# Performance work log

Measured on AMD Instinct MI355X. Metric: run time of the kernel, lower is better.

The kernel has to match this reference:

```python
import jax, jax.numpy as jnp
import numpy as np

N_AGENTS = 32
N_HEADS = 8
HEAD_DIM = 32          # atten_dim // n_heads
HID = 256              # rnn_hidden_dim
ATT = 256              # atten_dim
N_ACT = 32
NEG = -1e9             # finite stand-in for -inf; exp underflows to 0 in softmax


def setup_inputs() -> dict:
    key = jax.random.key(0)
    ks = jax.random.split(key, 20)
    B, N, E = 4096, 64, 128
    w = lambda k, shape: (jax.random.normal(k, shape, jnp.float32) * 0.05)
    return {
        "inputs": jax.random.normal(ks[0], (B, N, E), jnp.float32),
        "hidden_state": jax.random.normal(ks[1], (B, N_AGENTS, HID), jnp.float32) * 0.1,
        "fc1_w": w(ks[2], (HID, E)), "fc1_b": jnp.zeros((HID,), jnp.float32),
        "q_w": w(ks[3], (ATT, HID)), "q_b": jnp.zeros((ATT,), jnp.float32),
        "k_w": w(ks[4], (ATT, HID)), "k_b": jnp.zeros((ATT,), jnp.float32),
        "v_w": w(ks[5], (ATT, HID)), "v_b": jnp.zeros((ATT,), jnp.float32),
        "w_ih": w(ks[6], (3 * HID, ATT)), "w_hh": w(ks[7], (3 * HID, HID)),
        "b_ih": jnp.zeros((3 * HID,), jnp.float32), "b_hh": jnp.zeros((3 * HID,), jnp.float32),
        "out_w": w(ks[8], (N_ACT, HID)), "out_b": jnp.zeros((N_ACT,), jnp.float32),
        "obs_mask": jax.random.randint(ks[9], (B, N, N), 0, 2).astype(bool),
        "scenario_mask": jax.random.randint(ks[10], (B, N_AGENTS), 0, 2).astype(bool),
    }


def reference(inputs, hidden_state, fc1_w, fc1_b, q_w, q_b, k_w, k_b, v_w, v_b,
              w_ih, w_hh, b_ih, b_hh, out_w, out_b, obs_mask, scenario_mask):
    B, N, _ = inputs.shape
    A, nh, e = N_AGENTS, N_HEADS, HEAD_DIM
    # fc1 + ReLU: [B, N, HID]
    x = jax.nn.relu(inputs @ fc1_w.T + fc1_b)
    # multi-head projections; queries only for the first A entities (agents)
    q = (x[:, :A] @ q_w.T + q_b).reshape(B, A, nh, e).transpose(0, 2, 1, 3)   # [B,nh,A,e]
    k = (x @ k_w.T + k_b).reshape(B, N, nh, e).transpose(0, 2, 3, 1)          # [B,nh,e,N]
    v = jax.nn.relu(x @ v_w.T + v_b).reshape(B, N, nh, e).transpose(0, 2, 1, 3)  # [B,nh,N,e]
    score = jnp.einsum('bhae,bhen->bhan', q, k) / np.float32(np.sqrt(e))      # [B,nh,A,N]
    m = obs_mask[:, :A, :][:, None, :, :]                                      # [B,1,A,N]
    score = jnp.where(m, NEG, score)
    w = jax.nn.softmax(score, axis=-1)
    # original: fully-masked rows give NaN then are zeroed; here zero all masked slots
    w = jnp.where(m, 0.0, w)
    att = jnp.einsum('bhan,bhne->bhae', w, v)                                  # [B,nh,A,e]
    att = att.transpose(0, 2, 1, 3).reshape(B * A, nh * e)                     # [B*A, ATT]
    # GRUCell step (PyTorch gate ordering: r, z, n)
    h0 = hidden_state.reshape(B * A, HID)
    gi = att @ w_ih.T + b_ih
    gh = h0 @ w_hh.T + b_hh
    ir, iz, in_ = jnp.split(gi, 3, axis=-1)
    hr, hz, hn = jnp.split(gh, 3, axis=-1)
    r = jax.nn.sigmoid(ir + hr)
    z = jax.nn.sigmoid(iz + hz)
    n = jnp.tanh(in_ + r * hn)
    h = (1.0 - z) * n + z * h0
    h = h.reshape(B, A, HID)
    am = scenario_mask[:, :, None]                                             # [B,A,1]
    h = jnp.where(am, 0.0, h)
    q_out = h @ out_w.T + out_b
    q_out = jnp.where(am, 0.0, q_out)
    return q_out, h
```

## Files before the change

kernel.cpp:

```cpp
#include <hip/hip_runtime.h>


using bfrag = __attribute__((ext_vector_type(8))) short;
using ffrag = __attribute__((ext_vector_type(4))) float;

#define MFMA(a,b,c) __builtin_amdgcn_mfma_f32_16x16x32_bf16((a),(b),(c),0,0,0)
#define SWZ(row,col,S,xm) ((row)*(S) + ((((col)&~7) ^ (((row)&(xm))<<3)) | ((col)&7)))

#define OFF_A2   0L
#define OFF_FC1  67108864L
#define OFF_QW   67141632L
#define OFF_KW   67207168L
#define OFF_VW   67272704L
#define OFF_W6   67338240L
#define OFF_OW   67731456L
#define OFF_FLAG 67739648L
#define WS_NEED_BYTES 135479552L

__device__ inline unsigned short f2bf(float x){
  union { float f; unsigned u; } v; v.f = x;
  unsigned r = v.u + 0x7fffu + ((v.u >> 16) & 1u);
  return (unsigned short)(r >> 16);
}
__device__ inline bool getmask(const void* p, long i, int byteflag){
  return byteflag ? (((const unsigned char*)p)[i] != 0)
                  : (((const int*)p)[i] != 0);
}
__device__ inline ffrag fzero(){ ffrag z; z[0]=0.f; z[1]=0.f; z[2]=0.f; z[3]=0.f; return z; }
__device__ inline void gload16(const short* g, short* l){
  __builtin_amdgcn_global_load_lds((const __attribute__((address_space(1))) void*)g,
                                   (__attribute__((address_space(3))) void*)l, 16, 0, 0);
}
__device__ inline bfrag packbf(const float* p){
  float4 f0 = *(const float4*)p; float4 f1 = *(const float4*)(p+4);
  bfrag v;
  v[0]=(short)f2bf(f0.x); v[1]=(short)f2bf(f0.y); v[2]=(short)f2bf(f0.z); v[3]=(short)f2bf(f0.w);
  v[4]=(short)f2bf(f1.x); v[5]=(short)f2bf(f1.y); v[6]=(short)f2bf(f1.z); v[7]=(short)f2bf(f1.w);
  return v;
}

__global__ void k0_prep(const float* __restrict__ fc1, const float* __restrict__ qw,
    const float* __restrict__ kw, const float* __restrict__ vw, const float* __restrict__ wih,
    const float* __restrict__ whh, const float* __restrict__ ow,
    const void* __restrict__ obsm, short* __restrict__ ws){
  long tid = (long)blockIdx.x*blockDim.x + threadIdx.x;
  long n = (long)gridDim.x*blockDim.x;
  if (tid == 0){
    const int* mi = (const int*)obsm;
    int f = 0;
    for (int i=0;i<256;i++){ if ((unsigned)mi[i] > 1u){ f = 1; break; } }
    ((int*)(ws + OFF_FLAG))[0] = f;
  }
  for (long i=tid; i<32768; i+=n) ws[OFF_FC1+i] = (short)f2bf(fc1[i]);
  for (long i=tid; i<65536; i+=n){
    ws[OFF_QW+i] = (short)f2bf(qw[i]);
    ws[OFF_KW+i] = (short)f2bf(kw[i]);
    ws[OFF_VW+i] = (short)f2bf(vw[i]);
  }
  for (long i=tid; i<196608; i+=n){
    int gate = (int)(i >> 16);
    int grow = (int)((i >> 8) & 255);
    int c = (int)(i & 255);
    int jb = grow >> 5, row = grow & 31;
    int cs = c ^ ((row&7)<<3);
    ws[OFF_W6 + ((long)((jb*6 + gate)*32 + row))*256 + cs]     = (short)f2bf(wih[i]);
    ws[OFF_W6 + ((long)((jb*6 + 3 + gate)*32 + row))*256 + cs] = (short)f2bf(whh[i]);
  }
  for (long i=tid; i<8192; i+=n) ws[OFF_OW+i] = (short)f2bf(ow[i]);
}

__global__ __launch_bounds__(512) void k1_fqkv(const float* __restrict__ inp,
    const short* __restrict__ fc1B, const float* __restrict__ fc1_b,
    const short* __restrict__ wq, const short* __restrict__ wk, const short* __restrict__ wv,
    const float* __restrict__ qb, const float* __restrict__ kb, const float* __restrict__ vb,
    short* __restrict__ A2, short* __restrict__ kC, short* __restrict__ vC, int chunkB){
  __shared__ __align__(16) short smem[65536];
  short* a_s  = smem;
  short* fw_s = smem + 16384;
  short* x_s  = smem;
  int t = threadIdx.x;
  long R0 = (long)blockIdx.x * 128;
  long grow0 = (long)chunkB*131072 + R0;
  int lane = t&63, w = t>>6, lr = lane&15, ko = lane>>4;
  for (int i=0;i<4;i++){
    int c = t + i*512; int row = c>>4; int cc = (c&15)*8;
    *(bfrag*)(a_s + SWZ(row, cc, 128, 7)) = packbf(inp + (grow0 + row)*128 + cc);
  }
  for (int i=0;i<8;i++){
    int c = t + i*512; int row = c>>4; int cc = (c&15)*8;
    *(bfrag*)(fw_s + SWZ(row, cc, 128, 7)) = *(const bfrag*)(fc1B + row*128 + cc);
  }
  __syncthreads();
  ffrag acc1[16];
  #pragma unroll
  for (int i=0;i<16;i++) acc1[i]=fzero();
  for (int ks=0; ks<4; ks++){
    int kc = ks*32 + ko*8;
    bfrag a = *(const bfrag*)(a_s + SWZ(w*16+lr, kc, 128, 7));
    #pragma unroll
    for (int nt=0; nt<16; nt++){
      bfrag bb = *(const bfrag*)(fw_s + SWZ(nt*16+lr, kc, 128, 7));
      acc1[nt] = MFMA(a, bb, acc1[nt]);
    }
  }
  __syncthreads();
  #pragma unroll
  for (int nt=0; nt<16; nt++){
    float bias = fc1_b[nt*16+lr];
    #pragma unroll
    for (int r=0;r<4;r++){
      int row = w*16 + ko*4 + r;
      float v = acc1[nt][r] + bias; v = v>0.f?v:0.f;
      x_s[SWZ(row, nt*16+lr, 256, 7)] = (short)f2bf(v);
    }
  }
  __syncthreads();
  int rg = w & 3, chs = w >> 2;
  bfrag a_r[2][8];
  #pragma unroll
  for (int mt=0; mt<2; mt++)
    #pragma unroll
    for (int ks=0; ks<8; ks++)
      a_r[mt][ks] = *(const bfrag*)(x_s + SWZ(rg*32+mt*16+lr, ks*32+ko*8, 256, 7));
  auto STAGE2 = [&](int s){
    int kind = s>>2; int rb = (s&3)*64;
    const short* wsrc = (kind==0?wq:(kind==1?wk:wv)) + (long)rb*256;
    short* dst = smem + 32768 + (s&1)*16384;
    #pragma unroll
    for (int i=0;i<4;i++){
      int c = t + i*512; int row = c>>5; int cc = (c&31)*8;
      *(bfrag*)(dst + SWZ(row, cc, 256, 7)) = *(const bfrag*)(wsrc + (long)row*256 + cc);
    }
  };
  STAGE2(0);
  __syncthreads();
  for (int s=0; s<12; s++){
    if (s < 11) STAGE2(s+1);
    const short* wcur = smem + 32768 + (s&1)*16384;
    ffrag acc2[2][2];
    #pragma unroll
    for (int a=0;a<2;a++) for (int bq=0;bq<2;bq++) acc2[a][bq]=fzero();
    #pragma unroll
    for (int ks=0; ks<8; ks++){
      int kc = ks*32 + ko*8;
      #pragma unroll
      for (int ntl=0; ntl<2; ntl++){
        int ntc = chs*2 + ntl;
        bfrag bb = *(const bfrag*)(wcur + SWZ(ntc*16+lr, kc, 256, 7));
        acc2[0][ntl] = MFMA(a_r[0][ks], bb, acc2[0][ntl]);
        acc2[1][ntl] = MFMA(a_r[1][ks], bb, acc2[1][ntl]);
      }
    }
    int kind = s>>2; int rb = (s&3)*64;
    const float* bsrc = (kind==0?qb:(kind==1?kb:vb));
    #pragma unroll
    for (int mt=0; mt<2; mt++)
      #pragma unroll
      for (int ntl=0; ntl<2; ntl++){
        int colk = rb + (chs*2+ntl)*16 + lr;
        float bias = bsrc[colk];
        #pragma unroll
        for (int r=0;r<4;r++){
          int row = rg*32 + mt*16 + ko*4 + r;
          long rl = R0 + row;
          float v = acc2[mt][ntl][r] + bias;
          if (kind==0){
            if ((row&32)==0){
              long grow = grow0 + row;
              long qrow = ((grow>>6)<<5) + (grow&31);
              A2[qrow*256 + colk] = (short)f2bf(v);
            }
          } else if (kind==1){
            kC[rl*256 + colk] = (short)f2bf(v);
          } else {
            v = v>0.f?v:0.f;
            vC[rl*256 + colk] = (short)f2bf(v);
          }
        }
      }
    __syncthreads();
  }
}

__global__ __launch_bounds__(512,4) void k2_attn(const short* __restrict__ kC,
    const short* __restrict__ vC, const void* __restrict__ obsm, short* __restrict__ A2,
    const int* __restrict__ flagp, int chunkB){
  __shared__ __align__(16) short vT_s[8][2048];
  __shared__ __align__(16) short p_s[8][2048];
  __shared__ unsigned char m_s[2048];
  int t = threadIdx.x, bl = blockIdx.x;
  long b = (long)chunkB*2048 + bl;
  int lane = t&63, w = t>>6, lr = lane&15, ko = lane>>4;
  int mflag = *flagp;
  if (mflag){
    uchar4 mv = *(const uchar4*)((const unsigned char*)obsm + b*4096 + t*4);
    m_s[t*4]=mv.x; m_s[t*4+1]=mv.y; m_s[t*4+2]=mv.z; m_s[t*4+3]=mv.w;
  } else {
    int4 mv = *(const int4*)((const int*)obsm + b*4096 + t*4);
    m_s[t*4]  =(unsigned char)(mv.x!=0); m_s[t*4+1]=(unsigned char)(mv.y!=0);
    m_s[t*4+2]=(unsigned char)(mv.z!=0); m_s[t*4+3]=(unsigned char)(mv.w!=0);
  }
  const int h = w;
  const short* qh = A2 + ((long)b*32)*256 + h*32 + ko*8;
  bfrag a_q[2];
  #pragma unroll
  for (int mt=0; mt<2; mt++) a_q[mt] = *(const bfrag*)(qh + (long)(mt*16+lr)*256);
  const short* kh = kC + ((long)bl*64)*256 + h*32 + ko*8;
  bfrag b_k[4];
  #pragma unroll
  for (int nt=0; nt<4; nt++) b_k[nt] = *(const bfrag*)(kh + (nt*16+lr)*256);
  #pragma unroll
  for (int i=0;i<4;i++){
    int n = i*16 + (lane>>2); int e0 = (lane&3)*8;
    bfrag vv = *(const bfrag*)(vC + ((long)bl*64 + n)*256 + h*32 + e0);
    #pragma unroll
    for (int j=0;j<8;j++) vT_s[w][SWZ(e0+j, n, 64, 7)] = vv[j];
  }
  ffrag sc[2][4];
  #pragma unroll
  for (int mt=0; mt<2; mt++)
    #pragma unroll
    for (int nt=0; nt<4; nt++) sc[mt][nt] = MFMA(a_q[mt], b_k[nt], fzero());
  __syncthreads();
  const float scale = 0.17677669529663687f;
  float rsi[2][4];
  #pragma unroll
  for (int mt=0; mt<2; mt++){
    #pragma unroll
    for (int r=0; r<4; r++){
      int arow = mt*16 + ko*4 + r;
      float sv[4]; int mk[4];
      #pragma unroll
      for (int nt=0; nt<4; nt++){
        mk[nt] = m_s[arow*64 + nt*16 + lr];
        sv[nt] = sc[mt][nt][r] * scale;
      }
      float mx = -3.0e38f;
      #pragma unroll
      for (int nt=0; nt<4; nt++) if (!mk[nt]) mx = fmaxf(mx, sv[nt]);
      for (int d=1; d<16; d<<=1) mx = fmaxf(mx, __shfl_xor(mx, d));
      float sum = 0.f;
      #pragma unroll
      for (int nt=0; nt<4; nt++){
        float p = mk[nt] ? 0.f : __expf(sv[nt]-mx);
        sv[nt] = p; sum += p;
      }
      for (int d=1; d<16; d<<=1) sum += __shfl_xor(sum, d);
      rsi[mt][r] = sum > 0.f ? 1.f/sum : 0.f;
      #pragma unroll
      for (int nt=0; nt<4; nt++)
        p_s[w][SWZ(arow, nt*16+lr, 64, 7)] = (short)f2bf(sv[nt]);
    }
  }
  ffrag o[2][2];
  #pragma unroll
  for (int mt=0;mt<2;mt++)
    #pragma unroll
    for (int nt=0;nt<2;nt++) o[mt][nt]=fzero();
  #pragma unroll
  for (int kk=0; kk<2; kk++){
    int kc = kk*32 + ko*8;
    bfrag pa0 = *(const bfrag*)(p_s[w]  + SWZ(lr,    kc, 64, 7));
    bfrag pa1 = *(const bfrag*)(p_s[w]  + SWZ(16+lr, kc, 64, 7));
    bfrag bv0 = *(const bfrag*)(vT_s[w] + SWZ(lr,    kc, 64, 7));
    bfrag bv1 = *(const bfrag*)(vT_s[w] + SWZ(16+lr, kc, 64, 7));
    o[0][0]=MFMA(pa0,bv0,o[0][0]); o[0][1]=MFMA(pa0,bv1,o[0][1]);
    o[1][0]=MFMA(pa1,bv0,o[1][0]); o[1][1]=MFMA(pa1,bv1,o[1][1]);
  }
  #pragma unroll
  for (int mt=0; mt<2; mt++)
    #pragma unroll
    for (int nt=0; nt<2; nt++)
      #pragma unroll
      for (int r=0; r<4; r++){
        int a = mt*16 + ko*4 + r;
        A2[((long)b*32 + a)*256 + h*32 + nt*16 + lr] = (short)f2bf(o[mt][nt][r]*rsi[mt][r]);
      }
}

__global__ __launch_bounds__(512) void k3_gru(const short* __restrict__ A2,
    const float* __restrict__ h0f, const short* __restrict__ w6,
    const float* __restrict__ b_ih, const float* __restrict__ b_hh,
    const void* __restrict__ scen, float* __restrict__ hout, const int* __restrict__ flagp){
  __shared__ __align__(16) short w_s[2][16384];
  int t = threadIdx.x, bid = blockIdx.x;
  long R0 = (long)bid * 128;
  int mflag = *flagp;
  int lane = t&63, w = t>>6, lr = lane&15, ko = lane>>4;
  long rowbase = R0 + (long)w*16;
  auto STAGE = [&](int ph){
    const short* src = w6 + (long)ph*16384;
    short* dst = w_s[ph&1];
    #pragma unroll
    for (int i=0;i<4;i++)
      gload16(src + (long)(i*512 + t)*8, dst + (i*512 + (t & ~63))*8);
  };
  STAGE(0);
  const short* Ab = A2 + (rowbase + lr)*256 + ko*8;
  const float* Hb = h0f + (rowbase + lr)*256 + ko*8;
  bfrag A[16];
  #pragma unroll
  for (int ks=0; ks<8; ks++)
    A[ks] = *(const bfrag*)(Ab + ks*32);
  #pragma unroll
  for (int ks=0; ks<8; ks++)
    A[8+ks] = packbf(Hb + ks*32);
  __syncthreads();
  for (int jb=0; jb<8; jb++){
    ffrag aR[2], aZ[2], aI[2], aN[2];
    #pragma unroll
    for (int nt=0;nt<2;nt++){ aR[nt]=fzero(); aZ[nt]=fzero(); aI[nt]=fzero(); aN[nt]=fzero(); }
    #pragma unroll
    for (int p=0; p<3; p++){
      int ph = jb*3 + p;
      if (ph < 23) STAGE(ph+1);
      const short* wc = w_s[ph&1];
      #pragma unroll
      for (int ks=0; ks<8; ks++){
        int kc = ks*32 + ko*8;
        #pragma unroll
        for (int nt=0; nt<2; nt++){
          bfrag b0 = *(const bfrag*)(wc + SWZ(nt*16+lr, kc, 256, 7));
          bfrag b1 = *(const bfrag*)(wc + 8192 + SWZ(nt*16+lr, kc, 256, 7));
          if (p == 0){
            aR[nt] = MFMA(A[ks], b0, aR[nt]);
            aZ[nt] = MFMA(A[ks], b1, aZ[nt]);
          } else if (p == 1){
            aI[nt] = MFMA(A[ks], b0, aI[nt]);
            aR[nt] = MFMA(A[8+ks], b1, aR[nt]);
          } else {
            aZ[nt] = MFMA(A[8+ks], b0, aZ[nt]);
            aN[nt] = MFMA(A[8+ks], b1, aN[nt]);
          }
        }
      }
      if (p == 2){
        #pragma unroll
        for (int nt=0; nt<2; nt++){
          int j = jb*32 + nt*16 + lr;
          float bir = b_ih[j],     bhr = b_hh[j];
          float biz = b_ih[256+j], bhz = b_hh[256+j];
          float bin = b_ih[512+j], bhn = b_hh[512+j];
          #pragma unroll
          for (int rr=0; rr<4; rr++){
            long row = rowbase + ko*4 + rr;
            float rg = 1.f/(1.f + __expf(-(aR[nt][rr] + bir + bhr)));
            float zg = 1.f/(1.f + __expf(-(aZ[nt][rr] + biz + bhz)));
            float ag = aI[nt][rr] + bin + rg*(aN[nt][rr] + bhn);
            float ng = 2.f/(1.f + __expf(-2.f*ag)) - 1.f;
            float h0v = h0f[row*256 + j];
            float hv = (1.f - zg)*ng + zg*h0v;
            if (getmask(scen, row, mflag)) hv = 0.f;
            hout[row*256 + j] = hv;
          }
        }
      }
      __syncthreads();
    }
  }
}

__global__ __launch_bounds__(512) void k4_out(const float* __restrict__ hout,
    const short* __restrict__ ow, const float* __restrict__ out_b,
    const void* __restrict__ scen, float* __restrict__ qout, const int* __restrict__ flagp){
  __shared__ __align__(16) short ow_s[32*256];
  int t = threadIdx.x; long R0 = (long)blockIdx.x * 256;
  int mflag = *flagp;
  for (int i=0;i<2;i++){
    int c = t + i*512; int row = c >> 5; int cc = (c & 31)*8;
    *(bfrag*)(ow_s + SWZ(row, cc, 256, 7)) = *(const bfrag*)(ow + row*256 + cc);
  }
  __syncthreads();
  int lane = t&63, w = t>>6, lr = lane&15, ko = lane>>4;
  ffrag acc[2][2];
  #pragma unroll
  for (int a=0;a<2;a++) for (int bq=0;bq<2;bq++) acc[a][bq]=fzero();
  for (int ks=0; ks<8; ks++){
    int kc = ks*32 + ko*8;
    #pragma unroll
    for (int mi=0; mi<2; mi++){
      long row = R0 + (w*2+mi)*16 + lr;
      bfrag a = packbf(hout + row*256 + kc);
      #pragma unroll
      for (int nt=0; nt<2; nt++){
        bfrag bb = *(const bfrag*)(ow_s + SWZ(nt*16+lr, kc, 256, 7));
        acc[mi][nt] = MFMA(a, bb, acc[mi][nt]);
      }
    }
  }
  #pragma unroll
  for (int mi=0;mi<2;mi++)
    #pragma unroll
    for (int nt=0;nt<2;nt++){
      int col = nt*16 + lr;
      float ob = out_b[col];
      #pragma unroll
      for (int r=0;r<4;r++){
        long row = R0 + (w*2+mi)*16 + ko*4 + r;
        float qv = acc[mi][nt][r] + ob;
        if (getmask(scen, row, mflag)) qv = 0.f;
        qout[row*32 + col] = qv;
      }
    }
}

extern "C" void kernel_launch(void* const* d_in, const int* in_sizes, int n_in,
                              void* d_out, int out_size, void* d_ws, size_t ws_size,
                              hipStream_t stream){
  const float* inputs = (const float*)d_in[0];
  const float* hidden = (const float*)d_in[1];
  const float* fc1_w  = (const float*)d_in[2];
  const float* fc1_b  = (const float*)d_in[3];
  const float* q_w    = (const float*)d_in[4];
  const float* q_b    = (const float*)d_in[5];
  const float* k_w    = (const float*)d_in[6];
  const float* k_b    = (const float*)d_in[7];
  const float* v_w    = (const float*)d_in[8];
  const float* v_b    = (const float*)d_in[9];
  const float* w_ih   = (const float*)d_in[10];
  const float* w_hh   = (const float*)d_in[11];
  const float* b_ih   = (const float*)d_in[12];
  const float* b_hh   = (const float*)d_in[13];
  const float* out_w  = (const float*)d_in[14];
  const float* out_b  = (const float*)d_in[15];
  const void* obsm    = d_in[16];
  const void* scen    = d_in[17];
  (void)in_sizes; (void)n_in; (void)out_size;
  if ((long)ws_size < WS_NEED_BYTES) return;
  short* ws = (short*)d_ws;
  const int* flagp = (const int*)(ws + OFF_FLAG);
  float* qout = (float*)d_out;
  float* hout = qout + 4194304;
  short* kCs = (short*)hout;
  short* vCs = kCs + 33554432L;
  short* A2  = ws + OFF_A2;

  hipLaunchKernelGGL(k0_prep, dim3(512), dim3(256), 0, stream,
      fc1_w, q_w, k_w, v_w, w_ih, w_hh, out_w, obsm, ws);
  for (int c=0; c<2; c++){
    hipLaunchKernelGGL(k1_fqkv, dim3(1024), dim3(512), 0, stream,
        inputs, ws + OFF_FC1, fc1_b, ws + OFF_QW, ws + OFF_KW, ws + OFF_VW,
        q_b, k_b, v_b, A2, kCs, vCs, c);
    hipLaunchKernelGGL(k2_attn, dim3(2048), dim3(512), 0, stream,
        kCs, vCs, obsm, A2, flagp, c);
  }
  hipLaunchKernelGGL(k3_gru, dim3(1024), dim3(512), 0, stream,
      A2, hidden, ws + OFF_W6, b_ih, b_hh, scen, hout, flagp);
  hipLaunchKernelGGL(k4_out, dim3(512), dim3(512), 0, stream,
      hout, ws + OFF_OW, out_b, scen, qout, flagp);
}
```

Before: 614.3 us.

## Fuse fc1, QKV projection and attention into one per-batch kernel

Merges the fc1+QKV projection kernel and the attention kernel into a single kernel with one block per batch element. Q, K and V^T now stay in shared memory instead of round-tripping through a global K/V scratch buffer. Weights are pre-swizzled in the prep kernel and streamed into shared memory via double-buffered global_load_lds tiles. The trade-off is that each block re-streams all fc1/QKV weights for only 64 rows, so far more weight traffic goes through L2, and shared-memory use grows to about 148 KB per block, which limits occupancy.

```diff
diff --git a/kernel.cpp b/kernel.cpp
--- a/kernel.cpp
+++ b/kernel.cpp
@@ -9,9 +9,7 @@
 
 #define OFF_A2   0L
 #define OFF_FC1  67108864L
-#define OFF_QW   67141632L
-#define OFF_KW   67207168L
-#define OFF_VW   67272704L
+#define OFF_QKV  67141632L
 #define OFF_W6   67338240L
 #define OFF_OW   67731456L
 #define OFF_FLAG 67739648L
@@ -51,11 +49,18 @@
     for (int i=0;i<256;i++){ if ((unsigned)mi[i] > 1u){ f = 1; break; } }
     ((int*)(ws + OFF_FLAG))[0] = f;
   }
-  for (long i=tid; i<32768; i+=n) ws[OFF_FC1+i] = (short)f2bf(fc1[i]);
+  for (long i=tid; i<32768; i+=n){
+    int R = (int)(i>>7), c = (int)(i&127);
+    int seg = R>>6, r = R&63;
+    ws[OFF_FC1 + ((long)(seg*64+r)<<7) + (c ^ ((r&7)<<3))] = (short)f2bf(fc1[i]);
+  }
   for (long i=tid; i<65536; i+=n){
-    ws[OFF_QW+i] = (short)f2bf(qw[i]);
-    ws[OFF_KW+i] = (short)f2bf(kw[i]);
-    ws[OFF_VW+i] = (short)f2bf(vw[i]);
+    int R = (int)(i>>8), C = (int)(i&255);
+    int cb = R>>6, r = R&63, kh = C>>7, ck = C&127;
+    int cs = ck ^ ((r&7)<<3);
+    ws[OFF_QKV + ((long)(((0*4+cb)*2+kh)*64 + r)<<7) + cs] = (short)f2bf(qw[i]);
+    ws[OFF_QKV + ((long)(((1*4+cb)*2+kh)*64 + r)<<7) + cs] = (short)f2bf(kw[i]);
+    ws[OFF_QKV + ((long)(((2*4+cb)*2+kh)*64 + r)<<7) + cs] = (short)f2bf(vw[i]);
   }
   for (long i=tid; i<196608; i+=n){
     int gate = (int)(i >> 16);
@@ -69,213 +74,196 @@
   for (long i=tid; i<8192; i+=n) ws[OFF_OW+i] = (short)f2bf(ow[i]);
 }
 
-__global__ __launch_bounds__(512) void k1_fqkv(const float* __restrict__ inp,
-    const short* __restrict__ fc1B, const float* __restrict__ fc1_b,
-    const short* __restrict__ wq, const short* __restrict__ wk, const short* __restrict__ wv,
+__global__ __launch_bounds__(512) void k1_fused(const float* __restrict__ inp,
+    const short* __restrict__ fc1S, const float* __restrict__ fc1_b,
+    const short* __restrict__ qkvS,
     const float* __restrict__ qb, const float* __restrict__ kb, const float* __restrict__ vb,
-    short* __restrict__ A2, short* __restrict__ kC, short* __restrict__ vC, int chunkB){
-  __shared__ __align__(16) short smem[65536];
-  short* a_s  = smem;
-  short* fw_s = smem + 16384;
+    const void* __restrict__ obsm, short* __restrict__ A2, const int* __restrict__ flagp){
+  __shared__ __align__(16) short smem[75776];
   short* x_s  = smem;
-  int t = threadIdx.x;
-  long R0 = (long)blockIdx.x * 128;
-  long grow0 = (long)chunkB*131072 + R0;
-  int lane = t&63, w = t>>6, lr = lane&15, ko = lane>>4;
-  for (int i=0;i<4;i++){
-    int c = t + i*512; int row = c>>4; int cc = (c&15)*8;
-    *(bfrag*)(a_s + SWZ(row, cc, 128, 7)) = packbf(inp + (grow0 + row)*128 + cc);
-  }
-  for (int i=0;i<8;i++){
-    int c = t + i*512; int row = c>>4; int cc = (c&15)*8;
-    *(bfrag*)(fw_s + SWZ(row, cc, 128, 7)) = *(const bfrag*)(fc1B + row*128 + cc);
-  }
-  __syncthreads();
-  ffrag acc1[16];
-  #pragma unroll
-  for (int i=0;i<16;i++) acc1[i]=fzero();
-  for (int ks=0; ks<4; ks++){
-    int kc = ks*32 + ko*8;
-    bfrag a = *(const bfrag*)(a_s + SWZ(w*16+lr, kc, 128, 7));
-    #pragma unroll
-    for (int nt=0; nt<16; nt++){
-      bfrag bb = *(const bfrag*)(fw_s + SWZ(nt*16+lr, kc, 128, 7));
-      acc1[nt] = MFMA(a, bb, acc1[nt]);
-    }
-  }
-  __syncthreads();
-  #pragma unroll
-  for (int nt=0; nt<16; nt++){
-    float bias = fc1_b[nt*16+lr];
-    #pragma unroll
-    for (int r=0;r<4;r++){
-      int row = w*16 + ko*4 + r;
-      float v = acc1[nt][r] + bias; v = v>0.f?v:0.f;
-      x_s[SWZ(row, nt*16+lr, 256, 7)] = (short)f2bf(v);
-    }
-  }
-  __syncthreads();
-  int rg = w & 3, chs = w >> 2;
-  bfrag a_r[2][8];
-  #pragma unroll
-  for (int mt=0; mt<2; mt++)
-    #pragma unroll
-    for (int ks=0; ks<8; ks++)
-      a_r[mt][ks] = *(const bfrag*)(x_s + SWZ(rg*32+mt*16+lr, ks*32+ko*8, 256, 7));
-  auto STAGE2 = [&](int s){
-    int kind = s>>2; int rb = (s&3)*64;
-    const short* wsrc = (kind==0?wq:(kind==1?wk:wv)) + (long)rb*256;
-    short* dst = smem + 32768 + (s&1)*16384;
-    #pragma unroll
-    for (int i=0;i<4;i++){
-      int c = t + i*512; int row = c>>5; int cc = (c&31)*8;
-      *(bfrag*)(dst + SWZ(row, cc, 256, 7)) = *(const bfrag*)(wsrc + (long)row*256 + cc);
-    }
-  };
-  STAGE2(0);
-  __syncthreads();
-  for (int s=0; s<12; s++){
-    if (s < 11) STAGE2(s+1);
-    const short* wcur = smem + 32768 + (s&1)*16384;
-    ffrag acc2[2][2];
-    #pragma unroll
-    for (int a=0;a<2;a++) for (int bq=0;bq<2;bq++) acc2[a][bq]=fzero();
-    #pragma unroll
-    for (int ks=0; ks<8; ks++){
-      int kc = ks*32 + ko*8;
-      #pragma unroll
-      for (int ntl=0; ntl<2; ntl++){
-        int ntc = chs*2 + ntl;
-        bfrag bb = *(const bfrag*)(wcur + SWZ(ntc*16+lr, kc, 256, 7));
-        acc2[0][ntl] = MFMA(a_r[0][ks], bb, acc2[0][ntl]);
-        acc2[1][ntl] = MFMA(a_r[1][ks], bb, acc2[1][ntl]);
-      }
-    }
-    int kind = s>>2; int rb = (s&3)*64;
-    const float* bsrc = (kind==0?qb:(kind==1?kb:vb));
-    #pragma unroll
-    for (int mt=0; mt<2; mt++)
-      #pragma unroll
-      for (int ntl=0; ntl<2; ntl++){
-        int colk = rb + (chs*2+ntl)*16 + lr;
-        float bias = bsrc[colk];
-        #pragma unroll
-        for (int r=0;r<4;r++){
-          int row = rg*32 + mt*16 + ko*4 + r;
-          long rl = R0 + row;
-          float v = acc2[mt][ntl][r] + bias;
-          if (kind==0){
-            if ((row&32)==0){
-              long grow = grow0 + row;
-              long qrow = ((grow>>6)<<5) + (grow&31);
-              A2[qrow*256 + colk] = (short)f2bf(v);
-            }
-          } else if (kind==1){
-            kC[rl*256 + colk] = (short)f2bf(v);
-          } else {
-            v = v>0.f?v:0.f;
-            vC[rl*256 + colk] = (short)f2bf(v);
-          }
-        }
-      }
-    __syncthreads();
-  }
-}
-
-__global__ __launch_bounds__(512,4) void k2_attn(const short* __restrict__ kC,
-    const short* __restrict__ vC, const void* __restrict__ obsm, short* __restrict__ A2,
-    const int* __restrict__ flagp, int chunkB){
-  __shared__ __align__(16) short vT_s[8][2048];
-  __shared__ __align__(16) short p_s[8][2048];
-  __shared__ unsigned char m_s[2048];
-  int t = threadIdx.x, bl = blockIdx.x;
-  long b = (long)chunkB*2048 + bl;
+  short* wbuf = smem + 16384;
+  short* p_sb = smem + 16384;
+  short* a_s  = smem + 32768;
+  short* q_s  = smem + 32768;
+  short* k_s  = smem + 40960;
+  short* vT_s = smem + 57344;
+  unsigned char* m8 = (unsigned char*)(smem + 73728);
+  int t = threadIdx.x; int b = blockIdx.x;
   int lane = t&63, w = t>>6, lr = lane&15, ko = lane>>4;
   int mflag = *flagp;
+  auto STG = [&](const short* src, short* dst){
+    #pragma unroll
+    for (int i=0;i<2;i++)
+      gload16(src + (long)(i*512 + t)*8, dst + (i*512 + (t&~63))*8);
+  };
+  STG(fc1S, wbuf);
+  #pragma unroll
+  for (int i=0;i<2;i++){
+    int c = t + i*512; int row = c>>4; int cc = (c&15)*8;
+    *(bfrag*)(a_s + SWZ(row, cc, 128, 7)) = packbf(inp + ((long)b*64 + row)*128 + cc);
+  }
   if (mflag){
-    uchar4 mv = *(const uchar4*)((const unsigned char*)obsm + b*4096 + t*4);
-    m_s[t*4]=mv.x; m_s[t*4+1]=mv.y; m_s[t*4+2]=mv.z; m_s[t*4+3]=mv.w;
+    uchar4 mv = *(const uchar4*)((const unsigned char*)obsm + (long)b*4096 + t*4);
+    m8[t*4]=mv.x; m8[t*4+1]=mv.y; m8[t*4+2]=mv.z; m8[t*4+3]=mv.w;
   } else {
-    int4 mv = *(const int4*)((const int*)obsm + b*4096 + t*4);
-    m_s[t*4]  =(unsigned char)(mv.x!=0); m_s[t*4+1]=(unsigned char)(mv.y!=0);
-    m_s[t*4+2]=(unsigned char)(mv.z!=0); m_s[t*4+3]=(unsigned char)(mv.w!=0);
-  }
-  const int h = w;
-  const short* qh = A2 + ((long)b*32)*256 + h*32 + ko*8;
-  bfrag a_q[2];
-  #pragma unroll
-  for (int mt=0; mt<2; mt++) a_q[mt] = *(const bfrag*)(qh + (long)(mt*16+lr)*256);
-  const short* kh = kC + ((long)bl*64)*256 + h*32 + ko*8;
-  bfrag b_k[4];
-  #pragma unroll
-  for (int nt=0; nt<4; nt++) b_k[nt] = *(const bfrag*)(kh + (nt*16+lr)*256);
-  #pragma unroll
-  for (int i=0;i<4;i++){
-    int n = i*16 + (lane>>2); int e0 = (lane&3)*8;
-    bfrag vv = *(const bfrag*)(vC + ((long)bl*64 + n)*256 + h*32 + e0);
-    #pragma unroll
-    for (int j=0;j<8;j++) vT_s[w][SWZ(e0+j, n, 64, 7)] = vv[j];
-  }
-  ffrag sc[2][4];
-  #pragma unroll
-  for (int mt=0; mt<2; mt++)
-    #pragma unroll
-    for (int nt=0; nt<4; nt++) sc[mt][nt] = MFMA(a_q[mt], b_k[nt], fzero());
+    int4 mv = *(const int4*)((const int*)obsm + (long)b*4096 + t*4);
+    m8[t*4]  =(unsigned char)(mv.x!=0); m8[t*4+1]=(unsigned char)(mv.y!=0);
+    m8[t*4+2]=(unsigned char)(mv.z!=0); m8[t*4+3]=(unsigned char)(mv.w!=0);
+  }
   __syncthreads();
-  const float scale = 0.17677669529663687f;
-  float rsi[2][4];
-  #pragma unroll
-  for (int mt=0; mt<2; mt++){
-    #pragma unroll
-    for (int r=0; r<4; r++){
-      int arow = mt*16 + ko*4 + r;
-      float sv[4]; int mk[4];
-      #pragma unroll
-      for (int nt=0; nt<4; nt++){
-        mk[nt] = m_s[arow*64 + nt*16 + lr];
-        sv[nt] = sc[mt][nt][r] * scale;
-      }
-      float mx = -3.0e38f;
-      #pragma unroll
-      for (int nt=0; nt<4; nt++) if (!mk[nt]) mx = fmaxf(mx, sv[nt]);
-      for (int d=1; d<16; d<<=1) mx = fmaxf(mx, __shfl_xor(mx, d));
-      float sum = 0.f;
-      #pragma unroll
-      for (int nt=0; nt<4; nt++){
-        float p = mk[nt] ? 0.f : __expf(sv[nt]-mx);
-        sv[nt] = p; sum += p;
-      }
-      for (int d=1; d<16; d<<=1) sum += __shfl_xor(sum, d);
-      rsi[mt][r] = sum > 0.f ? 1.f/sum : 0.f;
-      #pragma unroll
-      for (int nt=0; nt<4; nt++)
-        p_s[w][SWZ(arow, nt*16+lr, 64, 7)] = (short)f2bf(sv[nt]);
-    }
-  }
-  ffrag o[2][2];
-  #pragma unroll
-  for (int mt=0;mt<2;mt++)
-    #pragma unroll
-    for (int nt=0;nt<2;nt++) o[mt][nt]=fzero();
-  #pragma unroll
-  for (int kk=0; kk<2; kk++){
-    int kc = kk*32 + ko*8;
-    bfrag pa0 = *(const bfrag*)(p_s[w]  + SWZ(lr,    kc, 64, 7));
-    bfrag pa1 = *(const bfrag*)(p_s[w]  + SWZ(16+lr, kc, 64, 7));
-    bfrag bv0 = *(const bfrag*)(vT_s[w] + SWZ(lr,    kc, 64, 7));
-    bfrag bv1 = *(const bfrag*)(vT_s[w] + SWZ(16+lr, kc, 64, 7));
-    o[0][0]=MFMA(pa0,bv0,o[0][0]); o[0][1]=MFMA(pa0,bv1,o[0][1]);
-    o[1][0]=MFMA(pa1,bv0,o[1][0]); o[1][1]=MFMA(pa1,bv1,o[1][1]);
-  }
-  #pragma unroll
-  for (int mt=0; mt<2; mt++)
-    #pragma unroll
-    for (int nt=0; nt<2; nt++)
+  {
+    int rg1 = w&3, ch1 = w>>2;
+    bfrag a1[4];
+    #pragma unroll
+    for (int ks=0;ks<4;ks++)
+      a1[ks] = *(const bfrag*)(a_s + SWZ(rg1*16+lr, ks*32+ko*8, 128, 7));
+    for (int s=0;s<4;s++){
+      STG((s<3) ? (fc1S + (s+1)*8192) : qkvS, wbuf + ((s+1)&1)*8192);
+      const short* wc = wbuf + (s&1)*8192;
+      ffrag acc[2]; acc[0]=fzero(); acc[1]=fzero();
+      #pragma unroll
+      for (int ks=0;ks<4;ks++){
+        int kc = ks*32+ko*8;
+        #pragma unroll
+        for (int nt=0;nt<2;nt++){
+          bfrag bb = *(const bfrag*)(wc + SWZ(ch1*32+nt*16+lr, kc, 128, 7));
+          acc[nt] = MFMA(a1[ks], bb, acc[nt]);
+        }
+      }
+      #pragma unroll
+      for (int nt=0;nt<2;nt++){
+        int colg = s*64 + ch1*32 + nt*16 + lr;
+        float bias = fc1_b[colg];
+        #pragma unroll
+        for (int r=0;r<4;r++){
+          int row = rg1*16 + ko*4 + r;
+          float v = acc[nt][r] + bias; v = v>0.f?v:0.f;
+          x_s[SWZ(row, colg, 256, 7)] = (short)f2bf(v);
+        }
+      }
+      __syncthreads();
+    }
+  }
+  {
+    int rg = w&1, chs = w>>1;
+    bfrag a_r[2][8];
+    #pragma unroll
+    for (int mt=0;mt<2;mt++)
+      #pragma unroll
+      for (int kk=0;kk<8;kk++)
+        a_r[mt][kk] = *(const bfrag*)(x_s + SWZ(rg*32+mt*16+lr, kk*32+ko*8, 256, 7));
+    ffrag acc[2];
+    for (int hs=0; hs<24; hs++){
+      if (hs<23) STG(qkvS + (long)(hs+1)*8192, wbuf + ((4+hs+1)&1)*8192);
+      int s12 = hs>>1, kh = hs&1;
+      int kind = s12>>2, cb = s12&3;
+      const short* wc = wbuf + ((4+hs)&1)*8192;
+      bool active = !(kind==0 && rg==1);
+      if (kh==0){ acc[0]=fzero(); acc[1]=fzero(); }
+      if (active){
+        #pragma unroll
+        for (int ks=0;ks<4;ks++){
+          int kc = ks*32+ko*8;
+          bfrag bb = *(const bfrag*)(wc + SWZ(chs*16+lr, kc, 128, 7));
+          acc[0] = MFMA(a_r[0][kh*4+ks], bb, acc[0]);
+          acc[1] = MFMA(a_r[1][kh*4+ks], bb, acc[1]);
+        }
+        if (kh==1){
+          int colg = cb*64 + chs*16 + lr;
+          float bias = (kind==0?qb:(kind==1?kb:vb))[colg];
+          #pragma unroll
+          for (int mt=0;mt<2;mt++){
+            #pragma unroll
+            for (int r=0;r<4;r++){
+              int row = rg*32 + mt*16 + ko*4 + r;
+              float v = acc[mt][r] + bias;
+              if (kind==0){
+                q_s[SWZ(row, colg, 256, 7)] = (short)f2bf(v);
+              } else if (kind==1){
+                k_s[SWZ(row, colg, 256, 7)] = (short)f2bf(v);
+              } else {
+                v = v>0.f?v:0.f;
+                int hh = colg>>5, e = colg&31;
+                vT_s[hh*2048 + SWZ(e, row, 64, 7)] = (short)f2bf(v);
+              }
+            }
+          }
+        }
+      }
+      __syncthreads();
+    }
+  }
+  {
+    const int h = w;
+    short* p_s = p_sb + h*2048;
+    bfrag a_q[2];
+    #pragma unroll
+    for (int mt=0; mt<2; mt++)
+      a_q[mt] = *(const bfrag*)(q_s + SWZ(mt*16+lr, h*32+ko*8, 256, 7));
+    bfrag b_k[4];
+    #pragma unroll
+    for (int nt=0; nt<4; nt++)
+      b_k[nt] = *(const bfrag*)(k_s + SWZ(nt*16+lr, h*32+ko*8, 256, 7));
+    ffrag sc[2][4];
+    #pragma unroll
+    for (int mt=0; mt<2; mt++)
+      #pragma unroll
+      for (int nt=0; nt<4; nt++) sc[mt][nt] = MFMA(a_q[mt], b_k[nt], fzero());
+    const float scale = 0.17677669529663687f;
+    float rsi[2][4];
+    #pragma unroll
+    for (int mt=0; mt<2; mt++){
       #pragma unroll
       for (int r=0; r<4; r++){
-        int a = mt*16 + ko*4 + r;
-        A2[((long)b*32 + a)*256 + h*32 + nt*16 + lr] = (short)f2bf(o[mt][nt][r]*rsi[mt][r]);
-      }
+        int arow = mt*16 + ko*4 + r;
+        float sv[4]; int mk[4];
+        #pragma unroll
+        for (int nt=0; nt<4; nt++){
+          mk[nt] = m8[arow*64 + nt*16 + lr];
+          sv[nt] = sc[mt][nt][r] * scale;
+        }
+        float mx = -3.0e38f;
+        #pragma unroll
+        for (int nt=0; nt<4; nt++) if (!mk[nt]) mx = fmaxf(mx, sv[nt]);
+        for (int d=1; d<16; d<<=1) mx = fmaxf(mx, __shfl_xor(mx, d));
+        float sum = 0.f;
+        #pragma unroll
+        for (int nt=0; nt<4; nt++){
+          float p = mk[nt] ? 0.f : __expf(sv[nt]-mx);
+          sv[nt] = p; sum += p;
+        }
+        for (int d=1; d<16; d<<=1) sum += __shfl_xor(sum, d);
+        rsi[mt][r] = sum > 0.f ? 1.f/sum : 0.f;
+        #pragma unroll
+        for (int nt=0; nt<4; nt++)
+          p_s[SWZ(arow, nt*16+lr, 64, 7)] = (short)f2bf(sv[nt]);
+      }
+    }
+    ffrag o[2][2];
+    #pragma unroll
+    for (int mt=0;mt<2;mt++)
+      #pragma unroll
+      for (int nt=0;nt<2;nt++) o[mt][nt]=fzero();
+    #pragma unroll
+    for (int kk=0; kk<2; kk++){
+      int kc = kk*32 + ko*8;
+      bfrag pa0 = *(const bfrag*)(p_s + SWZ(lr,    kc, 64, 7));
+      bfrag pa1 = *(const bfrag*)(p_s + SWZ(16+lr, kc, 64, 7));
+      bfrag bv0 = *(const bfrag*)(vT_s + h*2048 + SWZ(lr,    kc, 64, 7));
+      bfrag bv1 = *(const bfrag*)(vT_s + h*2048 + SWZ(16+lr, kc, 64, 7));
+      o[0][0]=MFMA(pa0,bv0,o[0][0]); o[0][1]=MFMA(pa0,bv1,o[0][1]);
+      o[1][0]=MFMA(pa1,bv0,o[1][0]); o[1][1]=MFMA(pa1,bv1,o[1][1]);
+    }
+    #pragma unroll
+    for (int mt=0; mt<2; mt++)
+      #pragma unroll
+      for (int nt=0; nt<2; nt++)
+        #pragma unroll
+        for (int r=0; r<4; r++){
+          int a = mt*16 + ko*4 + r;
+          A2[((long)b*32 + a)*256 + h*32 + nt*16 + lr] = (short)f2bf(o[mt][nt][r]*rsi[mt][r]);
+        }
+  }
 }
 
 __global__ __launch_bounds__(512) void k3_gru(const short* __restrict__ A2,
@@ -431,19 +419,12 @@
   const int* flagp = (const int*)(ws + OFF_FLAG);
   float* qout = (float*)d_out;
   float* hout = qout + 4194304;
-  short* kCs = (short*)hout;
-  short* vCs = kCs + 33554432L;
   short* A2  = ws + OFF_A2;
 
   hipLaunchKernelGGL(k0_prep, dim3(512), dim3(256), 0, stream,
       fc1_w, q_w, k_w, v_w, w_ih, w_hh, out_w, obsm, ws);
-  for (int c=0; c<2; c++){
-    hipLaunchKernelGGL(k1_fqkv, dim3(1024), dim3(512), 0, stream,
-        inputs, ws + OFF_FC1, fc1_b, ws + OFF_QW, ws + OFF_KW, ws + OFF_VW,
-        q_b, k_b, v_b, A2, kCs, vCs, c);
-    hipLaunchKernelGGL(k2_attn, dim3(2048), dim3(512), 0, stream,
-        kCs, vCs, obsm, A2, flagp, c);
-  }
+  hipLaunchKernelGGL(k1_fused, dim3(4096), dim3(512), 0, stream,
+      inputs, ws + OFF_FC1, fc1_b, ws + OFF_QKV, q_b, k_b, v_b, obsm, A2, flagp);
   hipLaunchKernelGGL(k3_gru, dim3(1024), dim3(512), 0, stream,
       A2, hidden, ws + OFF_W6, b_ih, b_hh, scen, hout, flagp);
   hipLaunchKernelGGL(k4_out, dim3(512), dim3(512), 0, stream,
```

New measurement: 557.2 us. 1.1x faster.
